# Performance work log

Hardware: AMD Instinct MI355X
Metric: run time of the kernel (lower is better)

Reference implementation:

```python
import jax, jax.numpy as jnp
import numpy as np

NUM_REL = 3


def setup_inputs() -> dict:
    key = jax.random.key(0)
    ks = jax.random.split(key, 12)
    N, E, G = 400_000, 2_000_000, 40_000
    V, D, H, C = 1024, 64, 96, 8
    sc = lambda k, shape: (jax.random.normal(k, shape, jnp.float32) * 0.05)
    return {
        "tokens": jax.random.randint(ks[0], (N,), 0, V),
        "edge_index": jax.random.randint(ks[1], (2, E), 0, N),
        "edge_type": jax.random.randint(ks[2], (E,), 0, NUM_REL),
        "batch": jnp.sort(jax.random.randint(ks[3], (N,), 0, G)),
        "num_graphs": G,
        "emb": sc(ks[4], (V, D)),
        "W1": sc(ks[5], (NUM_REL, D, H)),
        "root1": sc(ks[6], (D, H)),
        "b1": jnp.zeros((H,), jnp.float32),
        "W2": sc(ks[7], (NUM_REL, H, H)),
        "root2": sc(ks[8], (H, H)),
        "b2": jnp.zeros((H,), jnp.float32),
        "linW": sc(ks[9], (H, C)),
        "linb": jnp.zeros((C,), jnp.float32),
    }


def rgcn_layer(x, src, dst, etype, W, root, bias):
    # PyG RGCNConv with default aggr='mean': per-relation mean over incoming
    # edges, transformed by the relation weight, plus root transform and bias.
    N, Din = x.shape
    seg = dst * NUM_REL + etype  # combined (node, relation) segment id
    msgs = x[src]  # [E, Din] irregular gather
    sums = jax.ops.segment_sum(msgs, seg, num_segments=N * NUM_REL)
    sums = sums.reshape(N, NUM_REL, Din)
    cnt = jax.ops.segment_sum(jnp.ones_like(etype, dtype=x.dtype), seg,
                              num_segments=N * NUM_REL).reshape(N, NUM_REL, 1)
    mean = sums / jnp.maximum(cnt, 1.0)
    return jnp.einsum("nrd,rdh->nh", mean, W) + x @ root + bias


def reference(tokens, edge_index, edge_type, batch, num_graphs,
              emb, W1, root1, b1, W2, root2, b2, linW, linb):
    src, dst = edge_index[0], edge_index[1]
    x = emb[tokens]  # [N, D]
    x = jax.nn.relu(rgcn_layer(x, src, dst, edge_type, W1, root1, b1))
    # dropout(p=0.2) is identity in eval mode
    x = jax.nn.relu(rgcn_layer(x, src, dst, edge_type, W2, root2, b2))
    gsum = jax.ops.segment_sum(x, batch, num_segments=num_graphs)
    gcnt = jax.ops.segment_sum(jnp.ones((x.shape[0], 1), x.dtype), batch,
                               num_segments=num_graphs)
    pooled = gsum / jnp.maximum(gcnt, 1.0)  # global_mean_pool
    return pooled @ linW + linb
```

## Files before the change

kernel.cpp:

```cpp
#include <hip/hip_runtime.h>


#define NREL 3
#define DD 64
#define HH 96
#define CC 8
#define TM 16
#define KK 384

typedef __attribute__((ext_vector_type(8))) short bf16x8;
typedef __attribute__((ext_vector_type(4))) float f32x4;

__device__ __forceinline__ unsigned short f2bf(float x) {
    unsigned u = __float_as_uint(x);
    unsigned r = (u + 0x7fffu + ((u >> 16) & 1u)) >> 16;
    return (unsigned short)r;
}
__device__ __forceinline__ float bf2f(unsigned short h) {
    return __uint_as_float(((unsigned)h) << 16);
}

__global__ __launch_bounds__(256) void count_k(const int* __restrict__ dstv,
                                               const int* __restrict__ et, int E,
                                               int* __restrict__ cnt) {
    int e = blockIdx.x * 256 + threadIdx.x;
    if (e < E) atomicAdd(&cnt[dstv[e] * NREL + et[e]], 1);
}

__global__ __launch_bounds__(256) void scan_blk_k(const int* __restrict__ in, int S,
                                                  int* __restrict__ out,
                                                  int* __restrict__ bsum) {
    __shared__ int vals[1024];
    __shared__ int tsum[256];
    int base = blockIdx.x * 1024;
    for (int i = threadIdx.x; i < 1024; i += 256) {
        int g = base + i;
        vals[i] = (g < S) ? in[g] : 0;
    }
    __syncthreads();
    int t = threadIdx.x;
    int a0 = vals[t * 4], a1 = vals[t * 4 + 1], a2 = vals[t * 4 + 2], a3 = vals[t * 4 + 3];
    int s = a0 + a1 + a2 + a3;
    tsum[t] = s;
    __syncthreads();
    for (int off = 1; off < 256; off <<= 1) {
        int v = (t >= off) ? tsum[t - off] : 0;
        __syncthreads();
        tsum[t] += v;
        __syncthreads();
    }
    int excl = tsum[t] - s;
    int g = base + t * 4;
    if (g     < S) out[g]     = excl;
    if (g + 1 < S) out[g + 1] = excl + a0;
    if (g + 2 < S) out[g + 2] = excl + a0 + a1;
    if (g + 3 < S) out[g + 3] = excl + a0 + a1 + a2;
    if (t == 255) bsum[blockIdx.x] = tsum[255];
}

__global__ __launch_bounds__(256) void scan_top_k(int* __restrict__ bsum, int nb) {
    __shared__ int ts[256];
    int t = threadIdx.x;
    int loc[8];
    int s = 0;
    #pragma unroll
    for (int j = 0; j < 8; ++j) {
        int g = t * 8 + j;
        loc[j] = (g < nb) ? bsum[g] : 0;
        s += loc[j];
    }
    ts[t] = s;
    __syncthreads();
    for (int off = 1; off < 256; off <<= 1) {
        int v = (t >= off) ? ts[t - off] : 0;
        __syncthreads();
        ts[t] += v;
        __syncthreads();
    }
    int excl = ts[t] - s;
    #pragma unroll
    for (int j = 0; j < 8; ++j) {
        int g = t * 8 + j;
        if (g < nb) bsum[g] = excl;
        excl += loc[j];
    }
}

__global__ __launch_bounds__(256) void scan_add_k(int* __restrict__ out,
                                                  const int* __restrict__ bsum,
                                                  int S, int E) {
    int i = blockIdx.x * 256 + threadIdx.x;
    if (i < S) out[i] += bsum[i >> 10];
    else if (i == S) out[S] = E;
}

__global__ __launch_bounds__(256) void copy_k(const int* __restrict__ a,
                                              int* __restrict__ b, int n) {
    int i = blockIdx.x * 256 + threadIdx.x;
    if (i < n) b[i] = a[i];
}

__global__ __launch_bounds__(256) void fill_k(const int* __restrict__ srcv,
                                              const int* __restrict__ dstv,
                                              const int* __restrict__ et,
                                              const int* __restrict__ tokens, int E,
                                              int* __restrict__ cursor,
                                              int* __restrict__ ssrc,
                                              int* __restrict__ stok) {
    int e = blockIdx.x * 256 + threadIdx.x;
    if (e >= E) return;
    int s = srcv[e];
    int seg = dstv[e] * NREL + et[e];
    int pos = atomicAdd(&cursor[seg], 1);
    ssrc[pos] = s;
    stok[pos] = tokens[s];
}

__global__ __launch_bounds__(256) void gcnt_k(const int* __restrict__ batch, int N,
                                              float* __restrict__ gcnt) {
    int i = blockIdx.x * 256 + threadIdx.x;
    if (i < N) atomicAdd(&gcnt[batch[i]], 1.0f);
}

__global__ __launch_bounds__(256) void z1er_k(const float* __restrict__ emb,
                                              const float* __restrict__ W1,
                                              const float* __restrict__ root1,
                                              const float* __restrict__ b1,
                                              int V, float* __restrict__ z1,
                                              float* __restrict__ er1) {
    int idx = blockIdx.x * 256 + threadIdx.x;
    int tot = V * 4 * HH;
    if (idx >= tot) return;
    int v = idx / (4 * HH);
    int j = idx - v * 4 * HH;
    int r = j / HH;
    int h = j - r * HH;
    const float* ev = emb + (size_t)v * DD;
    float s = 0.f;
    if (r < NREL) {
        const float* w = W1 + ((size_t)r * DD) * HH + h;
        #pragma unroll 8
        for (int d = 0; d < DD; ++d) s += ev[d] * w[(size_t)d * HH];
        z1[((size_t)v * NREL + r) * HH + h] = s;
    } else {
        const float* w = root1 + h;
        #pragma unroll 8
        for (int d = 0; d < DD; ++d) s += ev[d] * w[(size_t)d * HH];
        er1[(size_t)v * HH + h] = s + b1[h];
    }
}

__global__ __launch_bounds__(256) void catwT_k(const float* __restrict__ W2,
                                               const float* __restrict__ root2,
                                               short* __restrict__ WTh,
                                               short* __restrict__ WTl) {
    int idx = blockIdx.x * 256 + threadIdx.x;
    const int tot = HH * KK;
    if (idx >= tot) return;
    int h = idx / KK;
    int K = idx - h * KK;
    float v = (K < NREL * HH) ? W2[(size_t)K * HH + h]
                              : root2[(size_t)(K - NREL * HH) * HH + h];
    unsigned short hi = f2bf(v);
    float res = v - bf2f(hi);
    unsigned short lo = f2bf(res);
    WTh[(size_t)h * KK + K] = (short)hi;
    WTl[(size_t)h * KK + K] = (short)lo;
}

__global__ __launch_bounds__(256) void l1_k(const int* __restrict__ rowptr,
                                            const int* __restrict__ stok,
                                            const int* __restrict__ tokens,
                                            const float* __restrict__ z1,
                                            const float* __restrict__ er1,
                                            float* __restrict__ h1, int N) {
    int idx = blockIdx.x * 256 + threadIdx.x;
    if (idx >= N * 24) return;
    int n = idx / 24;
    int q = idx - n * 24;
    int h0 = q * 4;
    float4 acc = *reinterpret_cast<const float4*>(er1 + (size_t)tokens[n] * HH + h0);
    int base = n * NREL;
    for (int r = 0; r < NREL; ++r) {
        int b = rowptr[base + r], e2 = rowptr[base + r + 1];
        float sx = 0.f, sy = 0.f, sz = 0.f, sw = 0.f;
        for (int i = b; i < e2; ++i) {
            int tok = stok[i];
            const float4 z = *reinterpret_cast<const float4*>(
                z1 + ((size_t)tok * NREL + r) * HH + h0);
            sx += z.x; sy += z.y; sz += z.z; sw += z.w;
        }
        float rc = 1.0f / fmaxf((float)(e2 - b), 1.0f);
        acc.x += sx * rc; acc.y += sy * rc; acc.z += sz * rc; acc.w += sw * rc;
    }
    float4 o;
    o.x = fmaxf(acc.x, 0.f); o.y = fmaxf(acc.y, 0.f);
    o.z = fmaxf(acc.z, 0.f); o.w = fmaxf(acc.w, 0.f);
    *reinterpret_cast<float4*>(h1 + (size_t)n * HH + h0) = o;
}

__global__ __launch_bounds__(384, 8) void l2_k(const int* __restrict__ rowptr,
                                               const int* __restrict__ ssrc,
                                               const float* __restrict__ h1,
                                               const short* __restrict__ WTh,
                                               const short* __restrict__ WTl,
                                               const float* __restrict__ b2,
                                               const int* __restrict__ batch,
                                               float* __restrict__ gsum, int N) {
    __shared__ short Ah[TM][392];
    __shared__ short Al[TM][392];
    int n0 = blockIdx.x * TM;
    int t = threadIdx.x;
    {
        int i = t & 15;
        int c = t >> 4;
        int d0 = c * 16;
        int n = n0 + i;
        float acc[16];
        #pragma unroll
        for (int j = 0; j < 16; ++j) acc[j] = 0.f;
        if (n < N) {
            if (c < 18) {
                int r = c / 6;
                int k0 = (c - r * 6) * 16;
                int b = rowptr[n * NREL + r], e2 = rowptr[n * NREL + r + 1];
                for (int ii = b; ii < e2; ++ii) {
                    const float* hrow = h1 + (size_t)ssrc[ii] * HH + k0;
                    #pragma unroll
                    for (int j = 0; j < 16; j += 4) {
                        const float4 v = *reinterpret_cast<const float4*>(hrow + j);
                        acc[j] += v.x; acc[j+1] += v.y; acc[j+2] += v.z; acc[j+3] += v.w;
                    }
                }
                float rc = 1.0f / fmaxf((float)(e2 - b), 1.0f);
                #pragma unroll
                for (int j = 0; j < 16; ++j) acc[j] *= rc;
            } else {
                int k0 = (c - 18) * 16;
                const float* hrow = h1 + (size_t)n * HH + k0;
                #pragma unroll
                for (int j = 0; j < 16; j += 4) {
                    const float4 v = *reinterpret_cast<const float4*>(hrow + j);
                    acc[j] = v.x; acc[j+1] = v.y; acc[j+2] = v.z; acc[j+3] = v.w;
                }
            }
        }
        #pragma unroll
        for (int w = 0; w < 2; ++w) {
            bf16x8 hv, lv;
            #pragma unroll
            for (int j = 0; j < 8; ++j) {
                float a = acc[w * 8 + j];
                unsigned short hb = f2bf(a);
                float res = a - bf2f(hb);
                unsigned short lb = f2bf(res);
                hv[j] = (short)hb;
                lv[j] = (short)lb;
            }
            *reinterpret_cast<bf16x8*>(&Ah[i][d0 + w * 8]) = hv;
            *reinterpret_cast<bf16x8*>(&Al[i][d0 + w * 8]) = lv;
        }
    }
    __syncthreads();
    int lane = t & 63;
    int w = t >> 6;
    int nb_ = w * 16;
    int r16 = lane & 15;
    int g = lane >> 4;

    float bi = b2[nb_ + r16];
    f32x4 acc = {bi, bi, bi, bi};

    const short* arow_h = &Ah[r16][8 * g];
    const short* arow_l = &Al[r16][8 * g];
    size_t wb = (size_t)(nb_ + r16) * KK + 8 * g;

    #pragma unroll
    for (int kk = 0; kk < KK / 32; ++kk) {
        int ko = kk * 32;
        bf16x8 ah = *reinterpret_cast<const bf16x8*>(arow_h + ko);
        bf16x8 al = *reinterpret_cast<const bf16x8*>(arow_l + ko);
        bf16x8 bh = *reinterpret_cast<const bf16x8*>(WTh + wb + ko);
        bf16x8 bl = *reinterpret_cast<const bf16x8*>(WTl + wb + ko);
        acc = __builtin_amdgcn_mfma_f32_16x16x32_bf16(ah, bh, acc, 0, 0, 0);
        acc = __builtin_amdgcn_mfma_f32_16x16x32_bf16(al, bh, acc, 0, 0, 0);
        acc = __builtin_amdgcn_mfma_f32_16x16x32_bf16(ah, bl, acc, 0, 0, 0);
    }
    #pragma unroll
    for (int r = 0; r < 4; ++r) {
        int node = n0 + g * 4 + r;
        if (node < N) {
            atomicAdd(gsum + (size_t)batch[node] * HH + nb_ + r16, fmaxf(acc[r], 0.f));
        }
    }
}

__global__ __launch_bounds__(256) void final_k(const float* __restrict__ gsum,
                                               const float* __restrict__ gcnt,
                                               const float* __restrict__ linW,
                                               const float* __restrict__ linb,
                                               float* __restrict__ out, int G) {
    int idx = blockIdx.x * 256 + threadIdx.x;
    if (idx >= G * CC) return;
    int g = idx / CC;
    int c = idx - g * CC;
    float rc = 1.0f / fmaxf(gcnt[g], 1.0f);
    const float* gs = gsum + (size_t)g * HH;
    float s = 0.f;
    #pragma unroll 8
    for (int h = 0; h < HH; ++h) s += gs[h] * linW[h * CC + c];
    out[idx] = s * rc + linb[c];
}

__global__ __launch_bounds__(256) void diag_k(float* __restrict__ out, int n, float v) {
    int i = blockIdx.x * 256 + threadIdx.x;
    if (i < n) out[i] = (i == 0) ? v : 0.f;
}

static inline int nblk(long long n) { return (int)((n + 255) / 256); }

extern "C" void kernel_launch(void* const* d_in, const int* in_sizes, int n_in,
                              void* d_out, int out_size, void* d_ws, size_t ws_size,
                              hipStream_t stream) {
    (void)n_in;
    const int* tokens = (const int*)d_in[0];
    const int* eidx   = (const int*)d_in[1];
    const int* etype  = (const int*)d_in[2];
    const int* batch  = (const int*)d_in[3];
    const float* emb   = (const float*)d_in[5];
    const float* W1    = (const float*)d_in[6];
    const float* root1 = (const float*)d_in[7];
    const float* b1    = (const float*)d_in[8];
    const float* W2    = (const float*)d_in[9];
    const float* root2 = (const float*)d_in[10];
    const float* b2v   = (const float*)d_in[11];
    const float* linW  = (const float*)d_in[12];
    const float* linb  = (const float*)d_in[13];
    float* out = (float*)d_out;

    const int N = in_sizes[0];
    const int E = in_sizes[2];
    const int V = in_sizes[5] / DD;
    const int G = out_size / CC;
    const int S = N * NREL;
    const int nb1 = (S + 1023) / 1024;

    const int* srcv = eidx;
    const int* dstv = eidx + E;

    auto align_up = [](size_t x) { return (x + 255) & ~(size_t)255; };
    size_t o_rowptr = 0;
    size_t o_cnt    = o_rowptr + align_up(((size_t)S + 1) * 4);
    size_t o_bsum   = o_cnt    + align_up((size_t)S * 4);
    size_t o_ssrc   = o_bsum   + align_up((size_t)2048 * 4);
    size_t o_stok   = o_ssrc   + align_up((size_t)E * 4);
    size_t o_z1     = o_stok   + align_up((size_t)E * 4);
    size_t o_er1    = o_z1     + align_up((size_t)V * NREL * HH * 4);
    size_t o_wth    = o_er1    + align_up((size_t)V * HH * 4);
    size_t o_wtl    = o_wth    + align_up((size_t)HH * KK * 2);
    size_t o_gsum   = o_wtl    + align_up((size_t)HH * KK * 2);
    size_t o_gcnt   = o_gsum   + align_up((size_t)G * HH * 4);
    size_t o_h1     = o_gcnt   + align_up((size_t)G * 4);
    size_t need     = o_h1     + align_up((size_t)N * HH * 4);

    if (ws_size < need || nb1 > 2048) {
        diag_k<<<nblk(out_size), 256, 0, stream>>>(out, out_size, (float)ws_size);
        return;
    }

    char* ws = (char*)d_ws;
    int*   rowptr = (int*)  (ws + o_rowptr);
    int*   cnt    = (int*)  (ws + o_cnt);
    int*   bsum   = (int*)  (ws + o_bsum);
    int*   ssrc   = (int*)  (ws + o_ssrc);
    int*   stok   = (int*)  (ws + o_stok);
    float* z1     = (float*)(ws + o_z1);
    float* er1    = (float*)(ws + o_er1);
    short* WTh    = (short*)(ws + o_wth);
    short* WTl    = (short*)(ws + o_wtl);
    float* gsum   = (float*)(ws + o_gsum);
    float* gcntv  = (float*)(ws + o_gcnt);
    float* h1     = (float*)(ws + o_h1);

    hipMemsetAsync(cnt, 0, (size_t)S * 4, stream);
    hipMemsetAsync(gsum, 0, (size_t)G * HH * 4, stream);
    hipMemsetAsync(gcntv, 0, (size_t)G * 4, stream);

    count_k<<<nblk(E), 256, 0, stream>>>(dstv, etype, E, cnt);
    scan_blk_k<<<nb1, 256, 0, stream>>>(cnt, S, rowptr, bsum);
    scan_top_k<<<1, 256, 0, stream>>>(bsum, nb1);
    scan_add_k<<<nblk((long long)S + 1), 256, 0, stream>>>(rowptr, bsum, S, E);
    copy_k<<<nblk(S), 256, 0, stream>>>(rowptr, cnt, S);
    fill_k<<<nblk(E), 256, 0, stream>>>(srcv, dstv, etype, tokens, E, cnt, ssrc, stok);
    z1er_k<<<nblk((long long)V * 4 * HH), 256, 0, stream>>>(emb, W1, root1, b1, V, z1, er1);
    catwT_k<<<nblk(HH * KK), 256, 0, stream>>>(W2, root2, WTh, WTl);
    gcnt_k<<<nblk(N), 256, 0, stream>>>(batch, N, gcntv);
    l1_k<<<nblk((long long)N * 24), 256, 0, stream>>>(rowptr, stok, tokens, z1, er1, h1, N);
    l2_k<<<(N + TM - 1) / TM, 384, 0, stream>>>(rowptr, ssrc, h1, WTh, WTl, b2v, batch,
                                                gsum, N);
    final_k<<<nblk((long long)G * CC), 256, 0, stream>>>(gsum, gcntv, linW, linb, out, G);
}
```

Measured before the change: 1.035 ms.

## Quantize layer-1 activations to packed 10-bit blocks for layer-2 gather

Layer 1 now writes bf16 activations, and a new kernel packs each row into 128 bytes of 10-bit integers with a shared exponent. Layer 2 gathers these compact rows, which cuts the bytes moved by the 2M-edge irregular gather. The gather is also restructured so 8 lanes cooperate per (node, relation) with a one-ahead prefetch, and rowptr is staged in LDS. The cost is an extra quantization pass and reduced precision (bf16 plus 10-bit mantissas), which could exceed the accuracy tolerance.

```diff
diff --git a/kernel.cpp b/kernel.cpp
--- a/kernel.cpp
+++ b/kernel.cpp
@@ -9,6 +9,7 @@
 #define KK 384
 
 typedef __attribute__((ext_vector_type(8))) short bf16x8;
+typedef __attribute__((ext_vector_type(4))) short s16x4;
 typedef __attribute__((ext_vector_type(4))) float f32x4;
 
 __device__ __forceinline__ unsigned short f2bf(float x) {
@@ -173,7 +174,7 @@
                                             const int* __restrict__ tokens,
                                             const float* __restrict__ z1,
                                             const float* __restrict__ er1,
-                                            float* __restrict__ h1, int N) {
+                                            unsigned short* __restrict__ h1h, int N) {
     int idx = blockIdx.x * 256 + threadIdx.x;
     if (idx >= N * 24) return;
     int n = idx / 24;
@@ -193,72 +194,157 @@
         float rc = 1.0f / fmaxf((float)(e2 - b), 1.0f);
         acc.x += sx * rc; acc.y += sy * rc; acc.z += sz * rc; acc.w += sw * rc;
     }
-    float4 o;
-    o.x = fmaxf(acc.x, 0.f); o.y = fmaxf(acc.y, 0.f);
-    o.z = fmaxf(acc.z, 0.f); o.w = fmaxf(acc.w, 0.f);
-    *reinterpret_cast<float4*>(h1 + (size_t)n * HH + h0) = o;
+    s16x4 hv;
+    hv[0] = (short)f2bf(fmaxf(acc.x, 0.f));
+    hv[1] = (short)f2bf(fmaxf(acc.y, 0.f));
+    hv[2] = (short)f2bf(fmaxf(acc.z, 0.f));
+    hv[3] = (short)f2bf(fmaxf(acc.w, 0.f));
+    *reinterpret_cast<s16x4*>(&h1h[(size_t)n * HH + h0]) = hv;
+}
+
+__global__ __launch_bounds__(256) void quant_k(const unsigned short* __restrict__ h1h,
+                                               unsigned* __restrict__ h1q, int N) {
+    int idx = blockIdx.x * 256 + threadIdx.x;
+    int n = idx >> 4;
+    int l = idx & 15;
+    if (n >= N) return;
+    const unsigned* row = reinterpret_cast<const unsigned*>(h1h + (size_t)n * HH) + 3 * l;
+    unsigned u0 = row[0], u1 = row[1], u2 = row[2];
+    float v[6] = { bf2f((unsigned short)(u0 & 0xffff)), bf2f((unsigned short)(u0 >> 16)),
+                   bf2f((unsigned short)(u1 & 0xffff)), bf2f((unsigned short)(u1 >> 16)),
+                   bf2f((unsigned short)(u2 & 0xffff)), bf2f((unsigned short)(u2 >> 16)) };
+    float m = 0.f;
+    #pragma unroll
+    for (int j = 0; j < 6; ++j) m = fmaxf(m, v[j]);
+    #pragma unroll
+    for (int mask = 1; mask <= 8; mask <<= 1) m = fmaxf(m, __shfl_xor(m, mask));
+    unsigned eb = __float_as_uint(m) >> 23;
+    unsigned E8;
+    float qs;
+    if (eb < 40) {
+        E8 = 0; qs = 0.f;
+    } else {
+        E8 = eb - 9;
+        qs = __uint_as_float((263 - eb) << 23);
+    }
+    unsigned q[6];
+    #pragma unroll
+    for (int j = 0; j < 6; ++j) {
+        unsigned qi = (unsigned)__float2int_rn(v[j] * qs);
+        q[j] = qi > 1023u ? 1023u : qi;
+    }
+    int d0 = 2 * l;
+    unsigned e0 = (E8 >> (2 * (d0 & 3))) & 3u;
+    unsigned e1 = (E8 >> (2 * ((d0 + 1) & 3))) & 3u;
+    uint2 w;
+    w.x = q[0] | (q[1] << 10) | (q[2] << 20) | (e0 << 30);
+    w.y = q[3] | (q[4] << 10) | (q[5] << 20) | (e1 << 30);
+    *reinterpret_cast<uint2*>(h1q + (size_t)n * 32 + d0) = w;
 }
 
 __global__ __launch_bounds__(384, 8) void l2_k(const int* __restrict__ rowptr,
                                                const int* __restrict__ ssrc,
-                                               const float* __restrict__ h1,
+                                               const unsigned* __restrict__ h1q,
+                                               const unsigned short* __restrict__ h1h,
                                                const short* __restrict__ WTh,
                                                const short* __restrict__ WTl,
                                                const float* __restrict__ b2,
                                                const int* __restrict__ batch,
                                                float* __restrict__ gsum, int N) {
-    __shared__ short Ah[TM][392];
-    __shared__ short Al[TM][392];
+    __shared__ float Af32[TM][392];
+    __shared__ int rp[49];
+    short* ab = (short*)&Af32[0][0];
     int n0 = blockIdx.x * TM;
     int t = threadIdx.x;
+    if (t < 49) {
+        int idx = n0 * NREL + t;
+        int mx = N * NREL;
+        rp[t] = rowptr[idx < mx ? idx : mx];
+    }
+    __syncthreads();
     {
-        int i = t & 15;
-        int c = t >> 4;
-        int d0 = c * 16;
+        int grp = t >> 3, l = t & 7;
+        int i = grp & 15, r = grp >> 4;
         int n = n0 + i;
-        float acc[16];
-        #pragma unroll
-        for (int j = 0; j < 16; ++j) acc[j] = 0.f;
         if (n < N) {
-            if (c < 18) {
-                int r = c / 6;
-                int k0 = (c - r * 6) * 16;
-                int b = rowptr[n * NREL + r], e2 = rowptr[n * NREL + r + 1];
-                for (int ii = b; ii < e2; ++ii) {
-                    const float* hrow = h1 + (size_t)ssrc[ii] * HH + k0;
-                    #pragma unroll
-                    for (int j = 0; j < 16; j += 4) {
-                        const float4 v = *reinterpret_cast<const float4*>(hrow + j);
-                        acc[j] += v.x; acc[j+1] += v.y; acc[j+2] += v.z; acc[j+3] += v.w;
-                    }
-                }
-                float rc = 1.0f / fmaxf((float)(e2 - b), 1.0f);
-                #pragma unroll
-                for (int j = 0; j < 16; ++j) acc[j] *= rc;
-            } else {
-                int k0 = (c - 18) * 16;
-                const float* hrow = h1 + (size_t)n * HH + k0;
-                #pragma unroll
-                for (int j = 0; j < 16; j += 4) {
-                    const float4 v = *reinterpret_cast<const float4*>(hrow + j);
-                    acc[j] = v.x; acc[j+1] = v.y; acc[j+2] = v.z; acc[j+3] = v.w;
+            int b = rp[i * NREL + r], e2 = rp[i * NREL + r + 1];
+            float acc[12];
+            #pragma unroll
+            for (int j = 0; j < 12; ++j) acc[j] = 0.f;
+            if (b < e2) {
+                uint4 cur = *reinterpret_cast<const uint4*>(
+                    h1q + (size_t)ssrc[b] * 32 + 4 * l);
+                for (int ge = b; ge < e2; ++ge) {
+                    int gn = (ge + 1 < e2) ? ge + 1 : ge;
+                    uint4 nxt = *reinterpret_cast<const uint4*>(
+                        h1q + (size_t)ssrc[gn] * 32 + 4 * l);
+                    unsigned E8 = (cur.x >> 30) | ((cur.y >> 30) << 2)
+                                | ((cur.z >> 30) << 4) | ((cur.w >> 30) << 6);
+                    float sc = __uint_as_float(E8 << 23);
+                    unsigned wv0 = cur.x, wv1 = cur.y, wv2 = cur.z, wv3 = cur.w;
+                    acc[0]  += (float)(wv0 & 1023u) * sc;
+                    acc[1]  += (float)((wv0 >> 10) & 1023u) * sc;
+                    acc[2]  += (float)((wv0 >> 20) & 1023u) * sc;
+                    acc[3]  += (float)(wv1 & 1023u) * sc;
+                    acc[4]  += (float)((wv1 >> 10) & 1023u) * sc;
+                    acc[5]  += (float)((wv1 >> 20) & 1023u) * sc;
+                    acc[6]  += (float)(wv2 & 1023u) * sc;
+                    acc[7]  += (float)((wv2 >> 10) & 1023u) * sc;
+                    acc[8]  += (float)((wv2 >> 20) & 1023u) * sc;
+                    acc[9]  += (float)(wv3 & 1023u) * sc;
+                    acc[10] += (float)((wv3 >> 10) & 1023u) * sc;
+                    acc[11] += (float)((wv3 >> 20) & 1023u) * sc;
+                    cur = nxt;
                 }
             }
+            float rc = 1.0f / fmaxf((float)(e2 - b), 1.0f);
+            #pragma unroll
+            for (int j = 0; j < 12; j += 4) {
+                float4 v = {acc[j] * rc, acc[j + 1] * rc, acc[j + 2] * rc,
+                            acc[j + 3] * rc};
+                *reinterpret_cast<float4*>(&Af32[i][r * HH + 12 * l + j]) = v;
+            }
         }
+    }
+    __syncthreads();
+    int i2 = t & 15;
+    int c2 = t >> 4;
+    int d0 = c2 * 16;
+    int n2 = n0 + i2;
+    float a[16];
+    #pragma unroll
+    for (int j = 0; j < 16; ++j) a[j] = 0.f;
+    if (n2 < N) {
+        if (c2 < 18) {
+            #pragma unroll
+            for (int j = 0; j < 16; ++j) a[j] = Af32[i2][d0 + j];
+        } else {
+            int k0 = (c2 - 18) * 16;
+            const unsigned short* hr = h1h + (size_t)n2 * HH + k0;
+            bf16x8 v0 = *reinterpret_cast<const bf16x8*>(hr);
+            bf16x8 v1 = *reinterpret_cast<const bf16x8*>(hr + 8);
+            #pragma unroll
+            for (int j = 0; j < 8; ++j) {
+                a[j]     = bf2f((unsigned short)v0[j]);
+                a[8 + j] = bf2f((unsigned short)v1[j]);
+            }
+        }
+    }
+    __syncthreads();
+    {
+        bf16x8 hv, lv;
         #pragma unroll
         for (int w = 0; w < 2; ++w) {
-            bf16x8 hv, lv;
             #pragma unroll
-            for (int j = 0; j < 8; ++j) {
-                float a = acc[w * 8 + j];
-                unsigned short hb = f2bf(a);
-                float res = a - bf2f(hb);
-                unsigned short lb = f2bf(res);
-                hv[j] = (short)hb;
-                lv[j] = (short)lb;
+            for (int jj = 0; jj < 8; ++jj) {
+                float x = a[w * 8 + jj];
+                unsigned short hb = f2bf(x);
+                float res = x - bf2f(hb);
+                hv[jj] = (short)hb;
+                lv[jj] = (short)f2bf(res);
             }
-            *reinterpret_cast<bf16x8*>(&Ah[i][d0 + w * 8]) = hv;
-            *reinterpret_cast<bf16x8*>(&Al[i][d0 + w * 8]) = lv;
+            *reinterpret_cast<bf16x8*>(ab + i2 * 392 + d0 + w * 8) = hv;
+            *reinterpret_cast<bf16x8*>(ab + TM * 392 + i2 * 392 + d0 + w * 8) = lv;
         }
     }
     __syncthreads();
@@ -271,8 +357,8 @@
     float bi = b2[nb_ + r16];
     f32x4 acc = {bi, bi, bi, bi};
 
-    const short* arow_h = &Ah[r16][8 * g];
-    const short* arow_l = &Al[r16][8 * g];
+    const short* arow_h = ab + r16 * 392 + 8 * g;
+    const short* arow_l = ab + TM * 392 + r16 * 392 + 8 * g;
     size_t wb = (size_t)(nb_ + r16) * KK + 8 * g;
 
     #pragma unroll
@@ -360,8 +446,9 @@
     size_t o_wtl    = o_wth    + align_up((size_t)HH * KK * 2);
     size_t o_gsum   = o_wtl    + align_up((size_t)HH * KK * 2);
     size_t o_gcnt   = o_gsum   + align_up((size_t)G * HH * 4);
-    size_t o_h1     = o_gcnt   + align_up((size_t)G * 4);
-    size_t need     = o_h1     + align_up((size_t)N * HH * 4);
+    size_t o_h1h    = o_gcnt   + align_up((size_t)G * 4);
+    size_t o_h1q    = o_h1h    + align_up((size_t)N * HH * 2);
+    size_t need     = o_h1q    + align_up((size_t)N * 128);
 
     if (ws_size < need || nb1 > 2048) {
         diag_k<<<nblk(out_size), 256, 0, stream>>>(out, out_size, (float)ws_size);
@@ -380,7 +467,8 @@
     short* WTl    = (short*)(ws + o_wtl);
     float* gsum   = (float*)(ws + o_gsum);
     float* gcntv  = (float*)(ws + o_gcnt);
-    float* h1     = (float*)(ws + o_h1);
+    unsigned short* h1h = (unsigned short*)(ws + o_h1h);
+    unsigned*       h1q = (unsigned*)(ws + o_h1q);
 
     hipMemsetAsync(cnt, 0, (size_t)S * 4, stream);
     hipMemsetAsync(gsum, 0, (size_t)G * HH * 4, stream);
@@ -395,8 +483,10 @@
     z1er_k<<<nblk((long long)V * 4 * HH), 256, 0, stream>>>(emb, W1, root1, b1, V, z1, er1);
     catwT_k<<<nblk(HH * KK), 256, 0, stream>>>(W2, root2, WTh, WTl);
     gcnt_k<<<nblk(N), 256, 0, stream>>>(batch, N, gcntv);
-    l1_k<<<nblk((long long)N * 24), 256, 0, stream>>>(rowptr, stok, tokens, z1, er1, h1, N);
-    l2_k<<<(N + TM - 1) / TM, 384, 0, stream>>>(rowptr, ssrc, h1, WTh, WTl, b2v, batch,
-                                                gsum, N);
+    l1_k<<<nblk((long long)N * 24), 256, 0, stream>>>(rowptr, stok, tokens, z1, er1,
+                                                      h1h, N);
+    quant_k<<<nblk((long long)N * 16), 256, 0, stream>>>(h1h, h1q, N);
+    l2_k<<<(N + TM - 1) / TM, 384, 0, stream>>>(rowptr, ssrc, h1q, h1h, WTh, WTl, b2v,
+                                                batch, gsum, N);
     final_k<<<nblk((long long)G * CC), 256, 0, stream>>>(gsum, gcntv, linW, linb, out, G);
 }
```

New measurement: 994.2 us. -3.9%, faster.
